# Kernel tuning notes

Hardware: AMD Instinct MI355X
Metric: run time of the kernel (lower is better)

## Reference

```python
import jax, jax.numpy as jnp
import numpy as np

N = 100000
E = 50000
NNZ = 1000000
IN_CH = 128
H = 8
C = 16
NEG_SLOPE = 0.2


def setup_inputs() -> dict:
    key = jax.random.key(0)
    ks = jax.random.split(key, 9)
    stdv_w = np.sqrt(6.0 / (IN_CH + H * C))
    stdv_a = np.sqrt(6.0 / (H + C))
    return {
        "X": jax.random.normal(ks[0], (N, IN_CH), dtype=jnp.float32),
        "W_w": jax.random.uniform(ks[1], (IN_CH, H * C), minval=-stdv_w, maxval=stdv_w, dtype=jnp.float32),
        "W_b": jnp.zeros((H * C,), dtype=jnp.float32),
        "att_e": jax.random.uniform(ks[2], (4, H, C), minval=-stdv_a, maxval=stdv_a, dtype=jnp.float32),
        "att_v": jax.random.uniform(ks[3], (4, H, C), minval=-stdv_a, maxval=stdv_a, dtype=jnp.float32),
        "vertex": jax.random.randint(ks[4], (NNZ,), 0, N, dtype=jnp.int32),
        "edges": jax.random.randint(ks[5], (NNZ,), 0, E, dtype=jnp.int32),
        "e_class": jax.random.randint(ks[6], (NNZ,), 0, 4, dtype=jnp.int32),
        "v_class": jax.random.randint(ks[7], (NNZ,), 0, 4, dtype=jnp.int32),
    }


def _leaky_relu(x):
    return jnp.where(x >= 0, x, NEG_SLOPE * x)


def _segment_softmax(x, seg, num_segments):
    # numerically stable softmax over segments (torch_geometric style)
    m = jax.ops.segment_max(x, seg, num_segments=num_segments)
    ex = jnp.exp(x - m[seg])
    s = jax.ops.segment_sum(ex, seg, num_segments=num_segments)
    return ex / (s[seg] + 1e-16)


def reference(X, W_w, W_b, att_e, att_v, vertex, edges, e_class, v_class):
    # X: [N, IN_CH] -> [N, H, C]
    Xn = (X @ W_w + W_b).reshape(N, H, C)
    Xve = Xn[vertex]                                  # [NNZ, H, C] gather

    # vertex -> edge attention (edge-type-specific attention vectors)
    beta = _leaky_relu((Xve * att_e[e_class]).sum(-1))  # [NNZ, H]
    beta = _segment_softmax(beta, edges, E)
    Xe = jax.ops.segment_sum(Xve * beta[..., None], edges, num_segments=E)  # [E, H, C]

    # edge -> vertex attention (node-type-specific attention vectors)
    Xev = Xe[edges]                                   # [NNZ, H, C] gather
    alpha = _leaky_relu((Xev * att_v[v_class]).sum(-1))  # [NNZ, H]
    alpha = _segment_softmax(alpha, vertex, N)
    Xv = jax.ops.segment_sum(Xev * alpha[..., None], vertex, num_segments=N)  # [N, H, C]

    return jax.nn.relu(Xv.reshape(N, H * C))
```

## Files before the change

kernel.cpp:

```cpp
#include <hip/hip_runtime.h>
#include <math.h>

#define NN 100000
#define EE 50000
#define ZZ 1000000

#define NB    196
#define SPB_E 256
#define SPB_V 512
#define IPB   4096
#define CAP   8192

#define PART_BLOCKS ((ZZ + IPB - 1) / IPB)
#define GEMM_BLOCKS ((NN + 63) / 64)
#define HIST_BLOCKS 512

typedef __attribute__((ext_vector_type(8))) short bf16x8;
typedef __attribute__((ext_vector_type(4))) float f32x4;

#if __has_builtin(__builtin_amdgcn_exp2f)
#define EXP2F(x) __builtin_amdgcn_exp2f(x)
#else
#define EXP2F(x) exp2f(x)
#endif
#if __has_builtin(__builtin_amdgcn_rcpf)
#define RCPF(x) __builtin_amdgcn_rcpf(x)
#else
#define RCPF(x) (1.f / (x))
#endif

__device__ __forceinline__ unsigned f2bf(float x) {
    const unsigned b = __float_as_uint(x);
    return (b + 0x7FFFu + ((b >> 16) & 1u)) >> 16;
}

__device__ __forceinline__ float xor1_add(float p) {
    return p + __int_as_float(__builtin_amdgcn_update_dpp(
        0, __float_as_int(p), 0xB1, 0xF, 0xF, true));
}

__global__ __launch_bounds__(256) void hist_wt(
    const int* __restrict__ vertex, const int* __restrict__ edges,
    unsigned* __restrict__ ghE, unsigned* __restrict__ ghV,
    const float* __restrict__ W, unsigned* __restrict__ Wtg)
{
    if (blockIdx.x >= HIST_BLOCKS) {
        const int b  = blockIdx.x - HIST_BLOCKS;
        const int n4 = threadIdx.x & 31;
        const int kp = b * 8 + (threadIdx.x >> 5);
        const float4* W4 = (const float4*)W;
        const float4 a = W4[(2 * kp) * 32 + n4];
        const float4 c = W4[(2 * kp + 1) * 32 + n4];
        Wtg[(4 * n4 + 0) * 68 + kp] = f2bf(a.x) | (f2bf(c.x) << 16);
        Wtg[(4 * n4 + 1) * 68 + kp] = f2bf(a.y) | (f2bf(c.y) << 16);
        Wtg[(4 * n4 + 2) * 68 + kp] = f2bf(a.z) | (f2bf(c.z) << 16);
        Wtg[(4 * n4 + 3) * 68 + kp] = f2bf(a.w) | (f2bf(c.w) << 16);
        return;
    }
    __shared__ unsigned hE[NB], hV[NB];
    for (int t = threadIdx.x; t < NB; t += 256) { hE[t] = 0; hV[t] = 0; }
    __syncthreads();
    const uint4* e4 = (const uint4*)edges;
    const uint4* v4 = (const uint4*)vertex;
    for (int i = blockIdx.x * 256 + threadIdx.x; i < ZZ / 4; i += HIST_BLOCKS * 256) {
        const uint4 e = e4[i];
        const uint4 v = v4[i];
        atomicAdd(&hE[e.x >> 8], 1u); atomicAdd(&hE[e.y >> 8], 1u);
        atomicAdd(&hE[e.z >> 8], 1u); atomicAdd(&hE[e.w >> 8], 1u);
        atomicAdd(&hV[v.x >> 9], 1u); atomicAdd(&hV[v.y >> 9], 1u);
        atomicAdd(&hV[v.z >> 9], 1u); atomicAdd(&hV[v.w >> 9], 1u);
    }
    __syncthreads();
    for (int t = threadIdx.x; t < NB; t += 256) {
        if (hE[t]) atomicAdd(&ghE[t], hE[t]);
        if (hV[t]) atomicAdd(&ghV[t], hV[t]);
    }
}

__device__ __forceinline__ void partition_body(
    unsigned* smem, int bid,
    const int* __restrict__ vertex, const int* __restrict__ edges,
    const int* __restrict__ ecl, const int* __restrict__ vcl,
    const unsigned* __restrict__ ghE, const unsigned* __restrict__ ghV,
    unsigned* __restrict__ gcE, unsigned* __restrict__ gcV,
    unsigned* __restrict__ partE, unsigned* __restrict__ partV)
{
    unsigned* curE  = smem;
    unsigned* curV  = smem + 256;
    unsigned* baseE = smem + 512;
    unsigned* baseV = smem + 768;
    unsigned* sh    = smem + 1024;
    const int t = threadIdx.x;

    unsigned g = (t < NB) ? ghE[t] : 0u;
    sh[t] = g; __syncthreads();
    for (int o = 1; o < 256; o <<= 1) {
        const unsigned u = (t >= o) ? sh[t - o] : 0u; __syncthreads();
        sh[t] += u; __syncthreads();
    }
    if (t < NB) baseE[t] = sh[t] - g;
    __syncthreads();
    g = (t < NB) ? ghV[t] : 0u;
    sh[t] = g; __syncthreads();
    for (int o = 1; o < 256; o <<= 1) {
        const unsigned u = (t >= o) ? sh[t - o] : 0u; __syncthreads();
        sh[t] += u; __syncthreads();
    }
    if (t < NB) baseV[t] = sh[t] - g;
    if (t < NB) { curE[t] = 0u; curV[t] = 0u; }
    __syncthreads();

    const int beg = bid * IPB;
    const int end = min(beg + IPB, ZZ);
    for (int i = beg + t; i < end; i += 256) {
        atomicAdd(&curE[((unsigned)edges[i]) >> 8], 1u);
        atomicAdd(&curV[((unsigned)vertex[i]) >> 9], 1u);
    }
    __syncthreads();
    for (int k = t; k < NB; k += 256) {
        unsigned c = curE[k];
        curE[k] = c ? (baseE[k] + atomicAdd(&gcE[k], c)) : 0u;
        c = curV[k];
        curV[k] = c ? (baseV[k] + atomicAdd(&gcV[k], c)) : 0u;
    }
    __syncthreads();
    for (int i = beg + t; i < end; i += 256) {
        const unsigned e = (unsigned)edges[i];
        const unsigned v = (unsigned)vertex[i];
        const unsigned pe = atomicAdd(&curE[e >> 8], 1u);
        partE[pe] = v | (((unsigned)ecl[i]) << 17) | ((e & 255u) << 19);
        const unsigned pv = atomicAdd(&curV[v >> 9], 1u);
        partV[pv] = e | (((unsigned)vcl[i]) << 17) | ((v & 511u) << 19);
    }
}

__device__ __forceinline__ void gemm_body(
    unsigned* smem, int bid,
    const float* __restrict__ X, const unsigned* __restrict__ Wtg,
    const float* __restrict__ Bb, unsigned* __restrict__ outb)
{
    unsigned* Wt = smem;
    unsigned* Xl = smem + 4608;
    const int tid = threadIdx.x;
    const int wid = tid >> 6, lane = tid & 63;
    const int l16 = lane & 15, kg = lane >> 4;

    f32x4 acc[8];
#pragma unroll
    for (int nt = 0; nt < 8; ++nt) acc[nt] = (f32x4){0.f, 0.f, 0.f, 0.f};

#pragma unroll
    for (int h = 0; h < 2; ++h) {
        {
            const uint4* Wg4 = (const uint4*)Wtg;
            uint4* Wl4 = (uint4*)Wt;
#pragma unroll
            for (int i = 0; i < 4; ++i) {
                const int k = i * 256 + tid;
                const int n = k >> 3, c = k & 7;
                Wl4[n * 9 + c] = Wg4[n * 17 + h * 8 + c];
            }
        }
        {
            const float4* X4 = (const float4*)X;
            const size_t base = (size_t)bid * 2048;
#pragma unroll
            for (int i = 0; i < 4; ++i) {
                const int k = i * 256 + tid;
                const int row = k >> 4, q = k & 15;
                float4 v = make_float4(0.f, 0.f, 0.f, 0.f);
                if (bid * 64 + row < NN) v = X4[base + row * 32 + h * 16 + q];
                Xl[row * 36 + 2 * q]     = f2bf(v.x) | (f2bf(v.y) << 16);
                Xl[row * 36 + 2 * q + 1] = f2bf(v.z) | (f2bf(v.w) << 16);
            }
        }
        __syncthreads();
#pragma unroll
        for (int kt = 0; kt < 2; ++kt) {
            const bf16x8 a = *(const bf16x8*)&Xl[(16 * wid + l16) * 36 + kt * 16 + kg * 4];
#pragma unroll
            for (int nt = 0; nt < 8; ++nt) {
                const bf16x8 b = *(const bf16x8*)&Wt[(nt * 16 + l16) * 36 + kt * 16 + kg * 4];
                acc[nt] = __builtin_amdgcn_mfma_f32_16x16x32_bf16(a, b, acc[nt], 0, 0, 0);
            }
        }
        __syncthreads();
    }

    short* Xs = (short*)smem;
#pragma unroll
    for (int nt = 0; nt < 8; ++nt) {
        const float bc = Bb[nt * 16 + l16];
#pragma unroll
        for (int r = 0; r < 4; ++r) {
            const int rl = 16 * wid + kg * 4 + r;
            Xs[rl * 136 + nt * 16 + l16] = (short)f2bf(acc[nt][r] + bc);
        }
    }
    {
        const uint2* Xu = (const uint2*)smem;
        uint2* O = (uint2*)outb;
        const int rbase = bid * 64 + 16 * wid;
#pragma unroll
        for (int i = 0; i < 8; ++i) {
            const int f = i * 64 + lane;
            const int row = f >> 5, col = f & 31;
            const int grow = rbase + row;
            if (grow < NN)
                O[(size_t)grow * 32 + col] = Xu[(16 * wid + row) * 34 + col];
        }
    }
}

__global__ __launch_bounds__(256) void gemm_part(
    const float* __restrict__ X, const unsigned* __restrict__ Wtg,
    const float* __restrict__ Bb, unsigned* __restrict__ outb,
    const int* __restrict__ vertex, const int* __restrict__ edges,
    const int* __restrict__ ecl, const int* __restrict__ vcl,
    const unsigned* __restrict__ ghE, const unsigned* __restrict__ ghV,
    unsigned* __restrict__ gcE, unsigned* __restrict__ gcV,
    unsigned* __restrict__ partE, unsigned* __restrict__ partV)
{
    __shared__ unsigned smem[6912];
    if (blockIdx.x < PART_BLOCKS)
        partition_body(smem, blockIdx.x, vertex, edges, ecl, vcl,
                       ghE, ghV, gcE, gcV, partE, partV);
    else
        gemm_body(smem, blockIdx.x - PART_BLOCKS, X, Wtg, Bb, outb);
}

__global__ __launch_bounds__(256) void csr_build2(
    const unsigned* __restrict__ partE, const unsigned* __restrict__ partV,
    const unsigned* __restrict__ ghE, const unsigned* __restrict__ ghV,
    unsigned* __restrict__ offsE, unsigned* __restrict__ offsV,
    unsigned* __restrict__ csrE, unsigned* __restrict__ csrV)
{
    __shared__ unsigned hist[SPB_V];
    __shared__ unsigned thr[256];
    __shared__ unsigned loc[CAP];
    __shared__ unsigned begS, cntS;
    const bool isV = blockIdx.x >= NB;
    const unsigned* gh   = isV ? ghV : ghE;
    const unsigned* part = isV ? partV : partE;
    unsigned* offs = isV ? offsV : offsE;
    unsigned* csr  = isV ? csrV : csrE;
    const int spb  = isV ? SPB_V : SPB_E;
    const int nseg = isV ? NN : EE;
    const int b    = isV ? (int)blockIdx.x - NB : (int)blockIdx.x;
    const int t = threadIdx.x;

    unsigned g = (t < NB) ? gh[t] : 0u;
    thr[t] = g; __syncthreads();
    for (int o = 1; o < 256; o <<= 1) {
        const unsigned u = (t >= o) ? thr[t - o] : 0u; __syncthreads();
        thr[t] += u; __syncthreads();
    }
    if (t == b) { begS = thr[t] - g; cntS = min(g, (unsigned)CAP); }
    __syncthreads();
    const unsigned beg = begS, cnt = cntS;

    for (int k = t; k < spb; k += 256) hist[k] = 0;
    __syncthreads();
    for (unsigned i = t; i < cnt; i += 256)
        atomicAdd(&hist[(part[beg + i] >> 19) & (spb - 1)], 1u);
    __syncthreads();
    const int EL = spb >> 8;
    unsigned v[2] = {0u, 0u};
    unsigned tsum = 0;
    for (int k = 0; k < EL; ++k) { v[k] = hist[t * EL + k]; tsum += v[k]; }
    thr[t] = tsum; __syncthreads();
    for (int o = 1; o < 256; o <<= 1) {
        const unsigned u = (t >= o) ? thr[t - o] : 0u; __syncthreads();
        thr[t] += u; __syncthreads();
    }
    unsigned run = thr[t] - tsum;
    for (int k = 0; k < EL; ++k) {
        const int s = t * EL + k;
        const int gs = b * spb + s;
        if (gs <= nseg) offs[gs] = beg + run;
        hist[s] = run;
        run += v[k];
    }
    __syncthreads();
    for (unsigned i = t; i < cnt; i += 256) {
        const unsigned r = part[beg + i];
        const unsigned p = atomicAdd(&hist[(r >> 19) & (spb - 1)], 1u);
        if (p < (unsigned)CAP)
            loc[p] = (r & 0x1FFFFu) | (((r >> 17) & 3u) << 27);
    }
    __syncthreads();
    for (unsigned i = t; i < cnt; i += 256) csr[beg + i] = loc[i];
}

template <bool BF16OUT>
__global__ __launch_bounds__(256) void seg_att(
    const unsigned char* __restrict__ sb, const unsigned* __restrict__ offs,
    const unsigned* __restrict__ csr, const float* __restrict__ att,
    void* __restrict__ dst, int nseg)
{
    __shared__ float4 attl[128];
    if (threadIdx.x < 128) {
        const float4 a = ((const float4*)att)[threadIdx.x];
        attl[threadIdx.x] = make_float4(a.x * 1.44269504f, a.y * 1.44269504f,
                                        a.z * 1.44269504f, a.w * 1.44269504f);
    }
    __syncthreads();
    const int lane = threadIdx.x & 63;
    const int qt   = lane >> 4;
    const int sl   = lane & 15;
    const int wseg = (blockIdx.x * 256 + threadIdx.x) >> 6;
    if (wseg >= nseg) return;
    const unsigned beg = offs[wseg], end = offs[wseg + 1];
    const unsigned sloff = (unsigned)(sl << 4);

    float s = 0.f;
    float a0 = 0.f, a1 = 0.f, a2 = 0.f, a3 = 0.f;
    float a4 = 0.f, a5 = 0.f, a6 = 0.f, a7 = 0.f;

    auto compute = [&](const uint4 u, const float4 avA, const float4 avB, bool valid) {
        const float x0 = __uint_as_float(u.x << 16);
        const float x1 = __uint_as_float(u.x & 0xFFFF0000u);
        const float x2 = __uint_as_float(u.y << 16);
        const float x3 = __uint_as_float(u.y & 0xFFFF0000u);
        const float x4 = __uint_as_float(u.z << 16);
        const float x5 = __uint_as_float(u.z & 0xFFFF0000u);
        const float x6 = __uint_as_float(u.w << 16);
        const float x7 = __uint_as_float(u.w & 0xFFFF0000u);
        float p = fmaf(x0, avA.x, fmaf(x1, avA.y, fmaf(x2, avA.z, fmaf(x3, avA.w,
                  fmaf(x4, avB.x, fmaf(x5, avB.y, fmaf(x6, avB.z, x7 * avB.w)))))));
        p = xor1_add(p);
        const float b = fmaxf(p, 0.2f * p);
        const float e = valid ? EXP2F(b) : 0.f;
        s += e;
        a0 = fmaf(x0, e, a0); a1 = fmaf(x1, e, a1);
        a2 = fmaf(x2, e, a2); a3 = fmaf(x3, e, a3);
        a4 = fmaf(x4, e, a4); a5 = fmaf(x5, e, a5);
        a6 = fmaf(x6, e, a6); a7 = fmaf(x7, e, a7);
    };

    unsigned jj = beg;
    for (; jj + 8 <= end; jj += 8) {
        const unsigned pk0 = csr[jj + qt];
        const unsigned pk1 = csr[jj + 4 + qt];
        const uint4 u0 = *(const uint4*)(sb + (((pk0 & 0x07FFFFFFu) << 8) | sloff));
        const uint4 u1 = *(const uint4*)(sb + (((pk1 & 0x07FFFFFFu) << 8) | sloff));
        const float4 A0 = attl[(pk0 >> 27) * 32 + 2 * sl];
        const float4 B0 = attl[(pk0 >> 27) * 32 + 2 * sl + 1];
        const float4 A1 = attl[(pk1 >> 27) * 32 + 2 * sl];
        const float4 B1 = attl[(pk1 >> 27) * 32 + 2 * sl + 1];
        compute(u0, A0, B0, true);
        compute(u1, A1, B1, true);
    }
    for (; jj + 4 <= end; jj += 4) {
        const unsigned pk = csr[jj + qt];
        const uint4 u = *(const uint4*)(sb + (((pk & 0x07FFFFFFu) << 8) | sloff));
        compute(u, attl[(pk >> 27) * 32 + 2 * sl],
                attl[(pk >> 27) * 32 + 2 * sl + 1], true);
    }
    if (jj < end) {
        const unsigned rem = end - jj;
        const unsigned j = min(jj + (unsigned)qt, end - 1);
        const unsigned pk = csr[j];
        const uint4 u = *(const uint4*)(sb + (((pk & 0x07FFFFFFu) << 8) | sloff));
        compute(u, attl[(pk >> 27) * 32 + 2 * sl],
                attl[(pk >> 27) * 32 + 2 * sl + 1], (unsigned)qt < rem);
    }

    s  += __shfl_xor(s, 16);  s  += __shfl_xor(s, 32);
    a0 += __shfl_xor(a0, 16); a0 += __shfl_xor(a0, 32);
    a1 += __shfl_xor(a1, 16); a1 += __shfl_xor(a1, 32);
    a2 += __shfl_xor(a2, 16); a2 += __shfl_xor(a2, 32);
    a3 += __shfl_xor(a3, 16); a3 += __shfl_xor(a3, 32);
    a4 += __shfl_xor(a4, 16); a4 += __shfl_xor(a4, 32);
    a5 += __shfl_xor(a5, 16); a5 += __shfl_xor(a5, 32);
    a6 += __shfl_xor(a6, 16); a6 += __shfl_xor(a6, 32);
    a7 += __shfl_xor(a7, 16); a7 += __shfl_xor(a7, 32);

    const float inv = RCPF(s + 1e-16f);
    if (qt == 0) {
        const float o0 = a0 * inv, o1 = a1 * inv, o2 = a2 * inv, o3 = a3 * inv;
        const float o4 = a4 * inv, o5 = a5 * inv, o6 = a6 * inv, o7 = a7 * inv;
        if (BF16OUT) {
            uint4 r;
            r.x = f2bf(o0) | (f2bf(o1) << 16);
            r.y = f2bf(o2) | (f2bf(o3) << 16);
            r.z = f2bf(o4) | (f2bf(o5) << 16);
            r.w = f2bf(o6) | (f2bf(o7) << 16);
            ((uint4*)dst)[(size_t)wseg * 16 + sl] = r;
        } else {
            float4* O = (float4*)dst;
            O[(size_t)wseg * 32 + 2 * sl] =
                make_float4(fmaxf(o0, 0.f), fmaxf(o1, 0.f),
                            fmaxf(o2, 0.f), fmaxf(o3, 0.f));
            O[(size_t)wseg * 32 + 2 * sl + 1] =
                make_float4(fmaxf(o4, 0.f), fmaxf(o5, 0.f),
                            fmaxf(o6, 0.f), fmaxf(o7, 0.f));
        }
    }
}

extern "C" void kernel_launch(void* const* d_in, const int* in_sizes, int n_in,
                              void* d_out, int out_size, void* d_ws, size_t ws_size,
                              hipStream_t stream) {
    const float* X    = (const float*)d_in[0];
    const float* Ww   = (const float*)d_in[1];
    const float* Wb   = (const float*)d_in[2];
    const float* attE = (const float*)d_in[3];
    const float* attV = (const float*)d_in[4];
    const int* vertex = (const int*)d_in[5];
    const int* edges  = (const int*)d_in[6];
    const int* ecls   = (const int*)d_in[7];
    const int* vcls   = (const int*)d_in[8];
    float* out = (float*)d_out;

    char* w = (char*)d_ws;
    unsigned* ghE   = (unsigned*)(w);
    unsigned* ghV   = (unsigned*)(w + 1024);
    unsigned* gcE   = (unsigned*)(w + 2048);
    unsigned* gcV   = (unsigned*)(w + 3072);
    unsigned* offsE = (unsigned*)(w + 6144);
    unsigned* offsV = (unsigned*)(w + 206848);
    unsigned* csrE  = (unsigned*)(w + 606976);
    unsigned* csrV  = (unsigned*)(w + 4606976);
    unsigned* partE = (unsigned*)(w + 8606976);
    unsigned* partV = (unsigned*)(w + 12606976);
    unsigned* Wtg   = (unsigned*)(w + 21500000);
    unsigned* Xnb   = (unsigned*)d_out;
    unsigned* Xeb   = (unsigned*)(w + 8606976);

    hipMemsetAsync(d_ws, 0, 4096, stream);

    hist_wt<<<HIST_BLOCKS + 8, 256, 0, stream>>>(vertex, edges, ghE, ghV, Ww, Wtg);
    gemm_part<<<PART_BLOCKS + GEMM_BLOCKS, 256, 0, stream>>>(
        X, Wtg, Wb, Xnb, vertex, edges, ecls, vcls, ghE, ghV, gcE, gcV, partE, partV);
    csr_build2<<<2 * NB, 256, 0, stream>>>(partE, partV, ghE, ghV,
                                           offsE, offsV, csrE, csrV);

    seg_att<true><<<(EE * 64 + 255) / 256, 256, 0, stream>>>(
        (const unsigned char*)Xnb, offsE, csrE, attE, Xeb, EE);

    seg_att<false><<<(NN * 64 + 255) / 256, 256, 0, stream>>>(
        (const unsigned char*)Xeb, offsV, csrV, attV, out, NN);
}
```

Before: 157.9 us.

## Software-pipeline segment gathers and pad attention LDS table; widen GEMM stores

Measured after the change: 158.7 us. About the same (+0.5%).

```diff
diff --git a/kernel.cpp b/kernel.cpp
--- a/kernel.cpp
+++ b/kernel.cpp
@@ -198,16 +198,16 @@
         }
     }
     {
-        const uint2* Xu = (const uint2*)smem;
-        uint2* O = (uint2*)outb;
+        const uint4* Xu = (const uint4*)smem;
+        uint4* O = (uint4*)outb;
         const int rbase = bid * 64 + 16 * wid;
 #pragma unroll
-        for (int i = 0; i < 8; ++i) {
+        for (int i = 0; i < 4; ++i) {
             const int f = i * 64 + lane;
-            const int row = f >> 5, col = f & 31;
+            const int row = f >> 4, col = f & 15;
             const int grow = rbase + row;
             if (grow < NN)
-                O[(size_t)grow * 32 + col] = Xu[(16 * wid + row) * 34 + col];
+                O[(size_t)grow * 16 + col] = Xu[(16 * wid + row) * 17 + col];
         }
     }
 }
@@ -298,10 +298,11 @@
     const unsigned* __restrict__ csr, const float* __restrict__ att,
     void* __restrict__ dst, int nseg)
 {
-    __shared__ float4 attl[128];
+    __shared__ float4 attl[132];
     if (threadIdx.x < 128) {
         const float4 a = ((const float4*)att)[threadIdx.x];
-        attl[threadIdx.x] = make_float4(a.x * 1.44269504f, a.y * 1.44269504f,
+        const int cl = threadIdx.x >> 5, q = threadIdx.x & 31;
+        attl[cl * 33 + q] = make_float4(a.x * 1.44269504f, a.y * 1.44269504f,
                                         a.z * 1.44269504f, a.w * 1.44269504f);
     }
     __syncthreads();
@@ -317,7 +318,12 @@
     float a0 = 0.f, a1 = 0.f, a2 = 0.f, a3 = 0.f;
     float a4 = 0.f, a5 = 0.f, a6 = 0.f, a7 = 0.f;
 
-    auto compute = [&](const uint4 u, const float4 avA, const float4 avB, bool valid) {
+    auto gat = [&](unsigned pk) -> uint4 {
+        return *(const uint4*)(sb + (((pk & 0x07FFFFFFu) << 8) | sloff));
+    };
+    auto compute = [&](const uint4 u, unsigned pk, bool valid) {
+        const float4 avA = attl[(pk >> 27) * 33 + 2 * sl];
+        const float4 avB = attl[(pk >> 27) * 33 + 2 * sl + 1];
         const float x0 = __uint_as_float(u.x << 16);
         const float x1 = __uint_as_float(u.x & 0xFFFF0000u);
         const float x2 = __uint_as_float(u.y << 16);
@@ -339,31 +345,40 @@
     };
 
     unsigned jj = beg;
-    for (; jj + 8 <= end; jj += 8) {
-        const unsigned pk0 = csr[jj + qt];
-        const unsigned pk1 = csr[jj + 4 + qt];
-        const uint4 u0 = *(const uint4*)(sb + (((pk0 & 0x07FFFFFFu) << 8) | sloff));
-        const uint4 u1 = *(const uint4*)(sb + (((pk1 & 0x07FFFFFFu) << 8) | sloff));
-        const float4 A0 = attl[(pk0 >> 27) * 32 + 2 * sl];
-        const float4 B0 = attl[(pk0 >> 27) * 32 + 2 * sl + 1];
-        const float4 A1 = attl[(pk1 >> 27) * 32 + 2 * sl];
-        const float4 B1 = attl[(pk1 >> 27) * 32 + 2 * sl + 1];
-        compute(u0, A0, B0, true);
-        compute(u1, A1, B1, true);
+    const unsigned npair = (end - beg) >> 3;
+    if (npair) {
+        unsigned pk0 = csr[jj + qt];
+        unsigned pk1 = csr[jj + 4 + qt];
+        uint4 u0 = gat(pk0);
+        uint4 u1 = gat(pk1);
+        unsigned npk0 = csr[min(jj + 8 + (unsigned)qt, (unsigned)(ZZ - 1))];
+        unsigned npk1 = csr[min(jj + 12 + (unsigned)qt, (unsigned)(ZZ - 1))];
+        for (unsigned it = 0; it + 1 < npair; ++it) {
+            const uint4 nu0 = gat(npk0);
+            const uint4 nu1 = gat(npk1);
+            const unsigned fj = jj + 16;
+            const unsigned fpk0 = csr[min(fj + (unsigned)qt, (unsigned)(ZZ - 1))];
+            const unsigned fpk1 = csr[min(fj + 4 + (unsigned)qt, (unsigned)(ZZ - 1))];
+            compute(u0, pk0, true);
+            compute(u1, pk1, true);
+            pk0 = npk0; pk1 = npk1;
+            u0 = nu0; u1 = nu1;
+            npk0 = fpk0; npk1 = fpk1;
+            jj += 8;
+        }
+        compute(u0, pk0, true);
+        compute(u1, pk1, true);
+        jj += 8;
     }
     for (; jj + 4 <= end; jj += 4) {
         const unsigned pk = csr[jj + qt];
-        const uint4 u = *(const uint4*)(sb + (((pk & 0x07FFFFFFu) << 8) | sloff));
-        compute(u, attl[(pk >> 27) * 32 + 2 * sl],
-                attl[(pk >> 27) * 32 + 2 * sl + 1], true);
+        compute(gat(pk), pk, true);
     }
     if (jj < end) {
         const unsigned rem = end - jj;
         const unsigned j = min(jj + (unsigned)qt, end - 1);
         const unsigned pk = csr[j];
-        const uint4 u = *(const uint4*)(sb + (((pk & 0x07FFFFFFu) << 8) | sloff));
-        compute(u, attl[(pk >> 27) * 32 + 2 * sl],
-                attl[(pk >> 27) * 32 + 2 * sl + 1], (unsigned)qt < rem);
+        compute(gat(pk), pk, (unsigned)qt < rem);
     }
 
     s  += __shfl_xor(s, 16);  s  += __shfl_xor(s, 32);
```
